# Performance work log

Measured on AMD Instinct MI355X. Metric: run time of the kernel, lower is better.

## Reference

```python
import math
import jax, jax.numpy as jnp
import numpy as np

B, C, H, W, R, P = 4, 64, 128, 128, 5, 8


def circular_sample(x, r):
    """Bilinear ring sampling, grid_sample(align_corners=True, padding_mode='zeros') equivalent.
    x: [B,C,H,W]; returns [B,H,W,C,P]."""
    Bx, Cx, Hx, Wx = x.shape
    angles = jnp.linspace(0.0, 2.0 * math.pi, P + 1)[:-1]
    di = r * jnp.sin(angles)  # row offsets [P]
    dj = r * jnp.cos(angles)  # col offsets [P]
    yy = jnp.arange(Hx, dtype=x.dtype)[:, None, None] + di[None, None, :]  # [H,1,P]
    xx = jnp.arange(Wx, dtype=x.dtype)[None, :, None] + dj[None, None, :]  # [1,W,P]
    yy = jnp.broadcast_to(yy, (Hx, Wx, P))
    xx = jnp.broadcast_to(xx, (Hx, Wx, P))
    y0 = jnp.floor(yy); x0 = jnp.floor(xx)
    wy = yy - y0; wx = xx - x0
    y0i = y0.astype(jnp.int32); x0i = x0.astype(jnp.int32)

    def gather(yi, xi):
        valid = ((yi >= 0) & (yi < Hx) & (xi >= 0) & (xi < Wx)).astype(x.dtype)
        yc = jnp.clip(yi, 0, Hx - 1)
        xc = jnp.clip(xi, 0, Wx - 1)
        return x[:, :, yc, xc] * valid  # [B,C,H,W,P], zeros padding

    v00 = gather(y0i, x0i)
    v01 = gather(y0i, x0i + 1)
    v10 = gather(y0i + 1, x0i)
    v11 = gather(y0i + 1, x0i + 1)
    out = (v00 * (1 - wy) * (1 - wx) + v01 * (1 - wy) * wx
           + v10 * wy * (1 - wx) + v11 * wy * wx)
    return jnp.transpose(out, (0, 2, 3, 1, 4))  # [B,H,W,C,P] -> channel-major, point-minor


def setup_inputs() -> dict:
    key = jax.random.key(0)
    ks = jax.random.split(key, 3)
    x = jax.random.normal(ks[0], (B, C, H, W), dtype=jnp.float32)
    CP = C * P
    W1 = jax.random.normal(ks[1], (R, CP, 64), dtype=jnp.float32) / np.sqrt(CP)
    b1 = jnp.zeros((R, 64), dtype=jnp.float32)
    g1 = jnp.ones((R, 64), dtype=jnp.float32)
    bt1 = jnp.zeros((R, 64), dtype=jnp.float32)
    W2 = jax.random.normal(ks[2], (R, 64, C), dtype=jnp.float32) / 8.0
    b2 = jnp.zeros((R, C), dtype=jnp.float32)
    return {"x": x, "W1": W1, "b1": b1, "g1": g1, "bt1": bt1, "W2": W2, "b2": b2}


def reference(x, W1, b1, g1, bt1, W2, b2):
    Bx, Cx, Hx, Wx = x.shape
    acc = jnp.zeros((Bx, Hx * Wx, Cx), dtype=x.dtype)
    for r in range(R):  # small fixed radius loop, matches module structure
        feat = circular_sample(x, float(r)).reshape(Bx, Hx * Wx, Cx * P)
        h = feat @ W1[r] + b1[r]
        mu = jnp.mean(h, axis=-1, keepdims=True)
        var = jnp.mean((h - mu) ** 2, axis=-1, keepdims=True)
        h = (h - mu) / jnp.sqrt(var + 1e-5) * g1[r] + bt1[r]
        h = jax.nn.gelu(h, approximate=False)  # torch nn.GELU default = exact erf
        acc = acc + h @ W2[r] + b2[r]
    wts = jax.nn.sigmoid(acc).reshape(Bx, Hx, Wx, Cx).transpose(0, 3, 1, 2)
    return x * wts
```

## Files before the change

### kernel.cpp

```cpp
#include <hip/hip_runtime.h>
#include <math.h>

namespace {
constexpr int Hh = 128, Ww = 128;
constexpr int NDCAP = 48;
constexpr int UROW  = 56;

using short8 = __attribute__((ext_vector_type(8))) short;
using f32x4  = __attribute__((ext_vector_type(4))) float;

__device__ __forceinline__ unsigned short f2bf(float f) {
    union { float f; unsigned int u; } v; v.f = f;
    unsigned int u = v.u;
    unsigned int r = (u + 0x7FFFu + ((u >> 16) & 1u)) >> 16;
    return (unsigned short)r;
}

union U8 { unsigned int d[4]; short8 s; };

constexpr size_t XBF_OFF  = 0;
constexpr size_t W1P_OFF  = 8388608;
constexpr size_t W2P_OFF  = W1P_OFF + (size_t)484 * 4096;
constexpr size_t META_OFF = W2P_OFF + 40960;
constexpr size_t UOFF_OFF = META_OFF + 64;
constexpr size_t WVEC_OFF = UOFF_OFF + 1152;
constexpr size_t WS_NEED  = WVEC_OFF + 7680;
}

__global__ void rrf_table(int* __restrict__ meta, int* __restrict__ uoff,
                          float* __restrict__ wvec)
{
    __shared__ float grid[5][81][8];
    __shared__ unsigned char keep[5][81];
    __shared__ short dofs[5][81];
    __shared__ int nds[5];

    const int t = threadIdx.x;
    for (int i = t; i < 5 * 81 * 8; i += 512) ((float*)grid)[i] = 0.f;
    for (int i = t; i < 5 * UROW; i += 512) uoff[i] = 0;
    __syncthreads();

    if (t < 40) {
        int r = t >> 3, p = t & 7;
        float ang = (float)p * 0.78539818525314331f;
        float si = (float)sin((double)ang);
        float co = (float)cos((double)ang);
        float di = (float)r * si;
        float dj = (float)r * co;
        float y0f = floorf(di), x0f = floorf(dj);
        float wy = di - y0f, wx = dj - x0f;
        int y0 = (int)y0f, x0 = (int)x0f;
        float tw[4] = {(1.f - wy) * (1.f - wx), (1.f - wy) * wx,
                       wy * (1.f - wx), wy * wx};
        int ty[4] = {y0, y0, y0 + 1, y0 + 1};
        int tx[4] = {x0, x0 + 1, x0, x0 + 1};
        #pragma unroll
        for (int q = 0; q < 4; ++q) {
            if (fabsf(tw[q]) < 1e-6f) continue;
            grid[r][(ty[q] + 4) * 9 + (tx[q] + 4)][p] = tw[q];
        }
    }
    __syncthreads();

    if (t < 405) {
        int r = t / 81, ci = t - r * 81;
        float mx = 0.f;
        #pragma unroll
        for (int p = 0; p < 8; ++p) mx = fmaxf(mx, fabsf(grid[r][ci][p]));
        keep[r][ci] = (mx > 1e-6f) ? 1 : 0;
    }
    __syncthreads();

    if (t < 5) {
        int nd = 0;
        for (int ci = 0; ci < 81; ++ci) {
            dofs[t][ci] = (short)nd;
            nd += keep[t][ci];
        }
        nds[t] = nd;
    }
    __syncthreads();

    if (t < 405) {
        int r = t / 81, ci = t - r * 81;
        if (keep[r][ci]) {
            int d = dofs[r][ci];
            int iy = ci / 9, ix = ci - iy * 9;
            uoff[r * UROW + d] = (iy * 24 + (ix - 4)) * 80;
            #pragma unroll
            for (int p = 0; p < 8; ++p)
                wvec[(r * NDCAP + d) * 8 + p] = grid[r][ci][p];
        }
    }
    if (t == 0) {
        int base = 0;
        for (int r = 0; r < 5; ++r) {
            int nd  = nds[r];
            int ndp = (nd + 3) & ~3;
            meta[r]      = ndp;
            meta[5 + r]  = base;
            meta[11 + r] = nd;
            base += ndp;
        }
        meta[10] = base;
    }
}

__global__ void rrf_pack(const float* __restrict__ W1, const float* __restrict__ W2,
                         const int* __restrict__ meta, const float* __restrict__ wvec,
                         unsigned short* __restrict__ w1p, unsigned short* __restrict__ w2p)
{
    int bb = blockIdx.x;
    if (bb < 480) {
        int gid  = bb * 256 + threadIdx.x;
        int lane = gid & 63;
        int t    = (gid >> 6) & 3;
        int cc   = (gid >> 8) & 1;
        int rd   = gid >> 9;
        int r = rd / NDCAP, d = rd % NDCAP;
        if (r >= 5 || d >= meta[r]) return;
        int TOTP  = meta[10];
        int chunk = cc * TOTP + meta[5 + r] + d;
        unsigned short* dst = w1p + ((size_t)(chunk * 4 + t) * 64 + lane) * 8;
        if (d >= meta[11 + r]) {
            short8 z = {0,0,0,0,0,0,0,0};
            *(short8*)dst = z;
            return;
        }
        int n = t * 16 + (lane & 15);
        int cbase = cc * 32 + ((lane >> 4) << 3);
        const float* wv  = wvec + (r * NDCAP + d) * 8;
        const float* w1r = W1 + (size_t)r * 512 * 64;
        short8 o;
        #pragma unroll
        for (int j = 0; j < 8; ++j) {
            int c = cbase + j;
            float acc = 0.f;
            #pragma unroll
            for (int p = 0; p < 8; ++p)
                acc = fmaf(wv[p], w1r[(c * 8 + p) * 64 + n], acc);
            o[j] = (short)f2bf(acc);
        }
        *(short8*)dst = o;
    } else {
        int i = (bb - 480) * 256 + threadIdx.x;
        if (i < 20480) {
            int j    = i & 7;
            int lane = (i >> 3) & 63;
            int kc2  = (i >> 9) & 1;
            int t    = (i >> 10) & 3;
            int r    = i >> 12;
            int n = kc2 * 32 + ((lane >> 4) << 3) + j;
            int m = t * 16 + (lane & 15);
            w2p[i] = f2bf(W2[(r * 64 + n) * 64 + m]);
        }
    }
}

__global__ void rrf_xpose(const float* __restrict__ x, unsigned short* __restrict__ xbf)
{
    __shared__ float tl[64][65];
    int b   = blockIdx.x >> 8;
    int px0 = (blockIdx.x & 255) * 64;
    int tx = threadIdx.x & 63, ty = threadIdx.x >> 6;
    #pragma unroll
    for (int i = 0; i < 16; ++i) {
        int c = i * 4 + ty;
        tl[c][tx] = x[(((size_t)b * 64 + c) << 14) + px0 + tx];
    }
    __syncthreads();
    #pragma unroll
    for (int i = 0; i < 16; ++i) {
        int px = i * 4 + ty;
        xbf[(((size_t)b << 14) + px0 + px) * 64 + tx] = f2bf(tl[tx][px]);
    }
}

#define LDA(K, CI) { const unsigned short* _q = ap + (size_t)(CI) * 2048 + (lane << 3);   \
    A##K[0] = *(const short8*)(_q);        A##K[1] = *(const short8*)(_q + 512);          \
    A##K[2] = *(const short8*)(_q + 1024); A##K[3] = *(const short8*)(_q + 1536); }

#define LDB(K, U) {                                                                       \
    B##K[0] = *(const short8*)(tb + ((U) + lb0));                                         \
    B##K[1] = *(const short8*)(tb + ((U) + lb1)); }

#define MF(K) {                                                                           \
    _Pragma("unroll")                                                                     \
    for (int _t = 0; _t < 4; ++_t) {                                                      \
        hv[_t][0] = __builtin_amdgcn_mfma_f32_16x16x32_bf16(A##K[_t], B##K[0], hv[_t][0], 0, 0, 0); \
        hv[_t][1] = __builtin_amdgcn_mfma_f32_16x16x32_bf16(A##K[_t], B##K[1], hv[_t][1], 0, 0, 0); \
    } }

__global__ __launch_bounds__(512, 2)
void rrf_stencil3(const float* __restrict__ x, const unsigned short* __restrict__ xbf,
                  const unsigned short* __restrict__ w1p, const unsigned short* __restrict__ w2p,
                  const int* __restrict__ meta, const int* __restrict__ uoff,
                  const float* __restrict__ b1v, const float* __restrict__ g1v,
                  const float* __restrict__ btv, const float* __restrict__ b2v,
                  float* __restrict__ out)
{
    __shared__ __align__(16) unsigned short tile[576 * 40];
    __shared__ int uo_lds[5 * UROW];
    __shared__ int meta_lds[16];

    const int tid  = threadIdx.x;
    const int w    = tid >> 6;
    const int lane = tid & 63;
    const int col  = lane & 15;
    const int g    = lane >> 4;

    const int bid = blockIdx.x;
    const int b   = bid >> 6;
    const int r0  = ((bid >> 3) & 7) * 16;
    const int c0  = (bid & 7) * 16;

    char* tb = (char*)tile;
    const int lb0 = ((2 * w + 0) * 24 + col + 4) * 80 + g * 16;
    const int lb1 = ((2 * w + 1) * 24 + col + 4) * 80 + g * 16;

    for (int s = tid; s < 5 * UROW; s += 512) uo_lds[s] = uoff[s];
    if (tid < 16) meta_lds[tid] = meta[tid];

    f32x4 acc2[4][2];
    #pragma unroll
    for (int t = 0; t < 4; ++t)
        #pragma unroll
        for (int q = 0; q < 2; ++q) acc2[t][q] = f32x4{0.f, 0.f, 0.f, 0.f};

    const int src0 = 32 * (g & 1) + col;
    const int src1 = src0 + 16;
    const bool ghi = (g >> 1) != 0;

    #pragma unroll 1
    for (int r = 0; r < 5; ++r) {
        f32x4 hv[4][2];
        #pragma unroll
        for (int t = 0; t < 4; ++t)
            #pragma unroll
            for (int q = 0; q < 2; ++q) hv[t][q] = f32x4{0.f, 0.f, 0.f, 0.f};

        #pragma unroll 1
        for (int cc = 0; cc < 2; ++cc) {
            __syncthreads();
            for (int s = tid; s < 576; s += 512) {
                int trow = s / 24, tcol = s - trow * 24;
                int row = r0 - 4 + trow, cg = c0 - 4 + tcol;
                bool valid = ((unsigned)row < 128u) && ((unsigned)cg < 128u);
                unsigned short* dst = tile + s * 40;
                if (valid) {
                    const unsigned short* src =
                        xbf + (((size_t)(b << 14)) + row * 128 + cg) * 64 + cc * 32;
                    #pragma unroll
                    for (int k = 0; k < 4; ++k)
                        *(short8*)(dst + k * 8) = *(const short8*)(src + k * 8);
                } else {
                    short8 z = {0, 0, 0, 0, 0, 0, 0, 0};
                    #pragma unroll
                    for (int k = 0; k < 4; ++k) *(short8*)(dst + k * 8) = z;
                }
            }
            __syncthreads();

            const int ndp  = __builtin_amdgcn_readfirstlane(meta_lds[r]);
            const int base = __builtin_amdgcn_readfirstlane(meta_lds[5 + r]);
            const int TOTP = __builtin_amdgcn_readfirstlane(meta_lds[10]);
            const unsigned short* ap = w1p + (size_t)(cc * TOTP + base) * 2048;
            const int* uo = uo_lds + r * UROW;

            short8 A0[4], A1[4], A2[4], A3[4];
            short8 B0[2], B1[2], B2[2], B3[2];
            LDA(0, 0) LDB(0, uo[0])
            LDA(1, 1) LDB(1, uo[1])
            LDA(2, 2) LDB(2, uo[2])
            LDA(3, 3) LDB(3, uo[3])
            int u0 = uo[4], u1 = uo[5], u2 = uo[6], u3 = uo[7];
            #pragma unroll 1
            for (int d = 0; d < ndp; d += 4) {
                MF(0) LDA(0, d + 4) LDB(0, u0)
                MF(1) LDA(1, d + 5) LDB(1, u1)
                MF(2) LDA(2, d + 6) LDB(2, u2)
                MF(3) LDA(3, d + 7) LDB(3, u3)
                u0 = uo[d + 8];  u1 = uo[d + 9];
                u2 = uo[d + 10]; u3 = uo[d + 11];
            }
        }

        float b1r[4][4], g1r[4][4], btr[4][4];
        #pragma unroll
        for (int t = 0; t < 4; ++t)
            #pragma unroll
            for (int e = 0; e < 4; ++e) {
                int n = t * 16 + g * 4 + e;
                b1r[t][e] = b1v[r * 64 + n];
                g1r[t][e] = g1v[r * 64 + n];
                btr[t][e] = btv[r * 64 + n];
            }

        #pragma unroll
        for (int q = 0; q < 2; ++q) {
            float hq[4][4];
            float s = 0.f;
            #pragma unroll
            for (int t = 0; t < 4; ++t)
                #pragma unroll
                for (int e = 0; e < 4; ++e) {
                    float v = hv[t][q][e] + b1r[t][e];
                    hq[t][e] = v;
                    s += v;
                }
            s += __shfl_xor(s, 16);
            s += __shfl_xor(s, 32);
            const float mu = s * 0.015625f;
            float s2 = 0.f;
            #pragma unroll
            for (int t = 0; t < 4; ++t)
                #pragma unroll
                for (int e = 0; e < 4; ++e) {
                    float dd = hq[t][e] - mu;
                    s2 = fmaf(dd, dd, s2);
                }
            s2 += __shfl_xor(s2, 16);
            s2 += __shfl_xor(s2, 32);
            const float rs = rsqrtf(s2 * 0.015625f + 1e-5f);

            unsigned int pk[4][2];
            #pragma unroll
            for (int t = 0; t < 4; ++t) {
                float ge[4];
                #pragma unroll
                for (int e = 0; e < 4; ++e) {
                    float v = (hq[t][e] - mu) * rs * g1r[t][e] + btr[t][e];
                    ge[e] = 0.5f * v * (1.f + erff(v * 0.70710678118654752f));
                }
                pk[t][0] = (unsigned int)f2bf(ge[0]) | ((unsigned int)f2bf(ge[1]) << 16);
                pk[t][1] = (unsigned int)f2bf(ge[2]) | ((unsigned int)f2bf(ge[3]) << 16);
            }

            #pragma unroll
            for (int kc2 = 0; kc2 < 2; ++kc2) {
                unsigned int d0a = (unsigned int)__shfl((int)pk[kc2 * 2][0],     src0);
                unsigned int d0b = (unsigned int)__shfl((int)pk[kc2 * 2 + 1][0], src0);
                unsigned int d1a = (unsigned int)__shfl((int)pk[kc2 * 2][1],     src0);
                unsigned int d1b = (unsigned int)__shfl((int)pk[kc2 * 2 + 1][1], src0);
                unsigned int d2a = (unsigned int)__shfl((int)pk[kc2 * 2][0],     src1);
                unsigned int d2b = (unsigned int)__shfl((int)pk[kc2 * 2 + 1][0], src1);
                unsigned int d3a = (unsigned int)__shfl((int)pk[kc2 * 2][1],     src1);
                unsigned int d3b = (unsigned int)__shfl((int)pk[kc2 * 2 + 1][1], src1);
                U8 u;
                u.d[0] = ghi ? d0b : d0a;
                u.d[1] = ghi ? d1b : d1a;
                u.d[2] = ghi ? d2b : d2a;
                u.d[3] = ghi ? d3b : d3a;
                const unsigned short* a2 = w2p + (size_t)r * 4096 + (size_t)lane * 8
                                         + (size_t)kc2 * 512;
                #pragma unroll
                for (int t = 0; t < 4; ++t) {
                    short8 a2f = *(const short8*)(a2 + (size_t)t * 1024);
                    acc2[t][q] = __builtin_amdgcn_mfma_f32_16x16x32_bf16(
                        a2f, u.s, acc2[t][q], 0, 0, 0);
                }
            }
        }
    }

    #pragma unroll
    for (int t = 0; t < 4; ++t) {
        #pragma unroll
        for (int e = 0; e < 4; ++e) {
            int m = t * 16 + g * 4 + e;
            float sb = b2v[m] + b2v[64 + m] + b2v[128 + m] + b2v[192 + m] + b2v[256 + m];
            #pragma unroll
            for (int q = 0; q < 2; ++q) {
                float a = acc2[t][q][e] + sb;
                float wts = 1.f / (1.f + expf(-a));
                size_t off = (((size_t)b * 64 + m) << 14)
                           + (size_t)(r0 + 2 * w + q) * 128 + (c0 + col);
                out[off] = x[off] * wts;
            }
        }
    }
}

__global__ void rrf_prepack(const float* __restrict__ W1, const float* __restrict__ W2,
                            unsigned short* __restrict__ w1p, unsigned short* __restrict__ w2p)
{
    int i = blockIdx.x * 256 + threadIdx.x;
    if (i < 163840) {
        int jq   = i & 7;
        int lane = (i >> 3) & 63;
        int kc   = (i >> 9) & 15;
        int t    = (i >> 13) & 3;
        int r    = i >> 15;
        int k = kc * 32 + ((lane >> 4) << 3) + jq;
        int n = t * 16 + (lane & 15);
        w1p[i] = f2bf(W1[(r * 512 + k) * 64 + n]);
    }
    if (i < 20480) {
        int jq   = i & 7;
        int lane = (i >> 3) & 63;
        int kc2  = (i >> 9) & 1;
        int t    = (i >> 10) & 3;
        int r    = i >> 12;
        int n = kc2 * 32 + ((lane >> 4) << 3) + jq;
        int m = t * 16 + (lane & 15);
        w2p[i] = f2bf(W2[(r * 64 + n) * 64 + m]);
    }
}

__global__ __launch_bounds__(256, 2)
void rrf_mfma(const float* __restrict__ x,
              const unsigned short* __restrict__ w1p, const unsigned short* __restrict__ w2p,
              const float* __restrict__ b1v, const float* __restrict__ g1v,
              const float* __restrict__ btv, const float* __restrict__ b2v,
              float* __restrict__ out)
{
    __shared__ unsigned short gbuf[4][16][72];

    const int tid  = threadIdx.x;
    const int w    = tid >> 6;
    const int lane = tid & 63;
    const int col  = lane & 15;
    const int g    = lane >> 4;

    const int bid  = blockIdx.x;
    const int b    = bid >> 8;
    const int rem  = bid & 255;
    const int irow = rem >> 1;
    const int j0   = (rem & 1) * 64;
    const int j    = j0 + w * 16 + col;

    const float fi = (float)irow;
    const float fj = (float)j;
    const float* xb = x + ((size_t)b << 20);

    f32x4 acc2[4] = {f32x4{0,0,0,0}, f32x4{0,0,0,0}, f32x4{0,0,0,0}, f32x4{0,0,0,0}};

    #pragma unroll 1
    for (int r = 0; r < 5; ++r) {
        int   o00[8], o01[8], o10[8], o11[8];
        float w00[8], w01[8], w10[8], w11[8];
        const float rf = (float)r;
        #pragma unroll
        for (int p = 0; p < 8; ++p) {
            float ang = (float)p * 0.78539818525314331f;
            float yy = fi + rf * sinf(ang);
            float xx = fj + rf * cosf(ang);
            float y0f = floorf(yy), x0f = floorf(xx);
            float wy = yy - y0f, wx = xx - x0f;
            int y0 = (int)y0f, x0i = (int)x0f;
            int y1 = y0 + 1,   x1  = x0i + 1;
            float m00 = (y0 >= 0 && y0 < Hh && x0i >= 0 && x0i < Ww) ? 1.f : 0.f;
            float m01 = (y0 >= 0 && y0 < Hh && x1  >= 0 && x1  < Ww) ? 1.f : 0.f;
            float m10 = (y1 >= 0 && y1 < Hh && x0i >= 0 && x0i < Ww) ? 1.f : 0.f;
            float m11 = (y1 >= 0 && y1 < Hh && x1  >= 0 && x1  < Ww) ? 1.f : 0.f;
            int y0c = y0 < 0 ? 0 : (y0 > Hh - 1 ? Hh - 1 : y0);
            int y1c = y1 < 0 ? 0 : (y1 > Hh - 1 ? Hh - 1 : y1);
            int x0c = x0i < 0 ? 0 : (x0i > Ww - 1 ? Ww - 1 : x0i);
            int x1c = x1 < 0 ? 0 : (x1 > Ww - 1 ? Ww - 1 : x1);
            w00[p] = (1.f - wy) * (1.f - wx) * m00;
            w01[p] = (1.f - wy) * wx * m01;
            w10[p] = wy * (1.f - wx) * m10;
            w11[p] = wy * wx * m11;
            o00[p] = (y0c * Ww + x0c) * 4;
            o01[p] = (y0c * Ww + x1c) * 4;
            o10[p] = (y1c * Ww + x0c) * 4;
            o11[p] = (y1c * Ww + x1c) * 4;
        }

        f32x4 hv[4] = {f32x4{0,0,0,0}, f32x4{0,0,0,0}, f32x4{0,0,0,0}, f32x4{0,0,0,0}};
        const unsigned short* abase0 = w1p + ((size_t)((r * 64) * 64 + lane)) * 8;
        #pragma unroll 2
        for (int kc = 0; kc < 16; ++kc) {
            const int c = (kc << 2) + g;
            const char* xp = (const char*)(xb + ((size_t)c << 14));
            short8 bfrag;
            #pragma unroll
            for (int p = 0; p < 8; ++p) {
                float v00 = *(const float*)(xp + o00[p]);
                float v01 = *(const float*)(xp + o01[p]);
                float v10 = *(const float*)(xp + o10[p]);
                float v11 = *(const float*)(xp + o11[p]);
                float v = w00[p] * v00;
                v = fmaf(w01[p], v01, v);
                v = fmaf(w10[p], v10, v);
                v = fmaf(w11[p], v11, v);
                bfrag[p] = (short)f2bf(v);
            }
            const unsigned short* ab = abase0 + (size_t)kc * 512;
            #pragma unroll
            for (int t = 0; t < 4; ++t) {
                short8 af = *(const short8*)(ab + (size_t)t * 8192);
                hv[t] = __builtin_amdgcn_mfma_f32_16x16x32_bf16(af, bfrag, hv[t], 0, 0, 0);
            }
        }

        const int nb = g << 2;
        float hq[4][4];
        float s = 0.f;
        #pragma unroll
        for (int t = 0; t < 4; ++t)
            #pragma unroll
            for (int q = 0; q < 4; ++q) {
                float hvq = hv[t][q] + b1v[r * 64 + t * 16 + nb + q];
                hq[t][q] = hvq;
                s += hvq;
            }
        s += __shfl_xor(s, 16);
        s += __shfl_xor(s, 32);
        const float mu = s * 0.015625f;
        float s2 = 0.f;
        #pragma unroll
        for (int t = 0; t < 4; ++t)
            #pragma unroll
            for (int q = 0; q < 4; ++q) {
                float d = hq[t][q] - mu;
                s2 = fmaf(d, d, s2);
            }
        s2 += __shfl_xor(s2, 16);
        s2 += __shfl_xor(s2, 32);
        const float rs = rsqrtf(s2 * 0.015625f + 1e-5f);

        #pragma unroll
        for (int t = 0; t < 4; ++t)
            #pragma unroll
            for (int q = 0; q < 4; ++q) {
                int n = t * 16 + nb + q;
                float v = (hq[t][q] - mu) * rs * g1v[r * 64 + n] + btv[r * 64 + n];
                hq[t][q] = 0.5f * v * (1.f + erff(v * 0.70710678118654752f));
            }
        #pragma unroll
        for (int t = 0; t < 4; ++t) {
            #pragma unroll
            for (int q2 = 0; q2 < 4; q2 += 2) {
                unsigned int u = (unsigned int)f2bf(hq[t][q2])
                               | ((unsigned int)f2bf(hq[t][q2 + 1]) << 16);
                *(unsigned int*)&gbuf[w][col][t * 16 + nb + q2] = u;
            }
        }

        const unsigned short* a2base = w2p + ((size_t)((r * 8) * 64 + lane)) * 8;
        #pragma unroll
        for (int kc2 = 0; kc2 < 2; ++kc2) {
            short8 bf2 = *(const short8*)&gbuf[w][col][kc2 * 32 + g * 8];
            const unsigned short* a2 = a2base + (size_t)kc2 * 512;
            #pragma unroll
            for (int t = 0; t < 4; ++t) {
                short8 a2f = *(const short8*)(a2 + (size_t)t * 1024);
                acc2[t] = __builtin_amdgcn_mfma_f32_16x16x32_bf16(a2f, bf2, acc2[t], 0, 0, 0);
            }
        }
    }

    #pragma unroll
    for (int t = 0; t < 4; ++t) {
        #pragma unroll
        for (int q = 0; q < 4; ++q) {
            int m = t * 16 + (g << 2) + q;
            float sb = b2v[m] + b2v[64 + m] + b2v[128 + m] + b2v[192 + m] + b2v[256 + m];
            float a = acc2[t][q] + sb;
            float wts = 1.f / (1.f + expf(-a));
            size_t off = (((size_t)b * 64 + m) << 14) + ((size_t)irow << 7) + j;
            out[off] = x[off] * wts;
        }
    }
}

extern "C" void kernel_launch(void* const* d_in, const int* in_sizes, int n_in,
                              void* d_out, int out_size, void* d_ws, size_t ws_size,
                              hipStream_t stream)
{
    const float* x  = (const float*)d_in[0];
    const float* W1 = (const float*)d_in[1];
    const float* b1 = (const float*)d_in[2];
    const float* g1 = (const float*)d_in[3];
    const float* bt = (const float*)d_in[4];
    const float* W2 = (const float*)d_in[5];
    const float* b2 = (const float*)d_in[6];
    float* outp = (float*)d_out;
    char* ws = (char*)d_ws;

    if (ws_size >= WS_NEED) {
        unsigned short* xbf = (unsigned short*)(ws + XBF_OFF);
        unsigned short* w1p = (unsigned short*)(ws + W1P_OFF);
        unsigned short* w2p = (unsigned short*)(ws + W2P_OFF);
        int*   meta  = (int*)(ws + META_OFF);
        int*   uoffp = (int*)(ws + UOFF_OFF);
        float* wvec  = (float*)(ws + WVEC_OFF);

        rrf_xpose<<<dim3(1024), dim3(256), 0, stream>>>(x, xbf);
        rrf_table<<<dim3(1), dim3(512), 0, stream>>>(meta, uoffp, wvec);
        rrf_pack<<<dim3(564), dim3(256), 0, stream>>>(W1, W2, meta, wvec, w1p, w2p);
        rrf_stencil3<<<dim3(256), dim3(512), 0, stream>>>(x, xbf, w1p, w2p, meta, uoffp,
                                                          b1, g1, bt, b2, outp);
    } else {
        unsigned short* w1p = (unsigned short*)d_ws;
        unsigned short* w2p = w1p + 163840;
        rrf_prepack<<<dim3(640), dim3(256), 0, stream>>>(W1, W2, w1p, w2p);
        rrf_mfma<<<dim3(1024), dim3(256), 0, stream>>>(x, w1p, w2p, b1, g1, bt, b2, outp);
    }
}
```

Before: 108.5 us.

## Split hidden dim across wave pairs, load both channel halves once, LDS GELU exchange

The stencil kernel now assigns each wave 4 pixel rows and half of the 64 hidden units, instead of 2 rows and all 64 units. Each W1 fragment is reused across 4 B tiles, which lowers per-wave global weight traffic. Both 32-channel halves of the input tile are loaded into LDS once up front, removing the per-radius reload and its barriers. LayerNorm statistics are combined across the wave pair through LDS using single-pass sum and sum-of-squares, and GELU outputs pass through an LDS buffer instead of lane shuffles. In exchange it uses more LDS, adds barriers per radius, and the E[x²]−mu² variance is less numerically robust.

New measurement: 98.65 us. -9.1%, faster.

```diff
diff --git a/kernel.cpp b/kernel.cpp
--- a/kernel.cpp
+++ b/kernel.cpp
@@ -15,8 +15,6 @@
     unsigned int r = (u + 0x7FFFu + ((u >> 16) & 1u)) >> 16;
     return (unsigned short)r;
 }
-
-union U8 { unsigned int d[4]; short8 s; };
 
 constexpr size_t XBF_OFF  = 0;
 constexpr size_t W1P_OFF  = 8388608;
@@ -176,30 +174,33 @@
     }
 }
 
-#define LDA(K, CI) { const unsigned short* _q = ap + (size_t)(CI) * 2048 + (lane << 3);   \
-    A##K[0] = *(const short8*)(_q);        A##K[1] = *(const short8*)(_q + 512);          \
-    A##K[2] = *(const short8*)(_q + 1024); A##K[3] = *(const short8*)(_q + 1536); }
-
-#define LDB(K, U) {                                                                       \
+#define LDA4(K, CI) { const unsigned short* _q = ap + (size_t)(CI) * 2048 + tpoff + (lane << 3); \
+    A##K[0] = *(const short8*)(_q); A##K[1] = *(const short8*)(_q + 512); }
+
+#define LDB4(K, U) {                                                                      \
     B##K[0] = *(const short8*)(tb + ((U) + lb0));                                         \
-    B##K[1] = *(const short8*)(tb + ((U) + lb1)); }
-
-#define MF(K) {                                                                           \
+    B##K[1] = *(const short8*)(tb + ((U) + lb1));                                         \
+    B##K[2] = *(const short8*)(tb + ((U) + lb2));                                         \
+    B##K[3] = *(const short8*)(tb + ((U) + lb3)); }
+
+#define MF4(K) {                                                                          \
     _Pragma("unroll")                                                                     \
-    for (int _t = 0; _t < 4; ++_t) {                                                      \
-        hv[_t][0] = __builtin_amdgcn_mfma_f32_16x16x32_bf16(A##K[_t], B##K[0], hv[_t][0], 0, 0, 0); \
-        hv[_t][1] = __builtin_amdgcn_mfma_f32_16x16x32_bf16(A##K[_t], B##K[1], hv[_t][1], 0, 0, 0); \
+    for (int _q = 0; _q < 4; ++_q) {                                                      \
+        hv[0][_q] = __builtin_amdgcn_mfma_f32_16x16x32_bf16(A##K[0], B##K[_q], hv[0][_q], 0, 0, 0); \
+        hv[1][_q] = __builtin_amdgcn_mfma_f32_16x16x32_bf16(A##K[1], B##K[_q], hv[1][_q], 0, 0, 0); \
     } }
 
 __global__ __launch_bounds__(512, 2)
-void rrf_stencil3(const float* __restrict__ x, const unsigned short* __restrict__ xbf,
+void rrf_stencil4(const float* __restrict__ x, const unsigned short* __restrict__ xbf,
                   const unsigned short* __restrict__ w1p, const unsigned short* __restrict__ w2p,
                   const int* __restrict__ meta, const int* __restrict__ uoff,
                   const float* __restrict__ b1v, const float* __restrict__ g1v,
                   const float* __restrict__ btv, const float* __restrict__ b2v,
                   float* __restrict__ out)
 {
-    __shared__ __align__(16) unsigned short tile[576 * 40];
+    __shared__ __align__(16) unsigned short tile[2][23040];
+    __shared__ __align__(16) unsigned short gbuf[16][16][72];
+    __shared__ float wsum[2][4][4][16][2];
     __shared__ int uo_lds[5 * UROW];
     __shared__ int meta_lds[16];
 
@@ -208,157 +209,171 @@
     const int lane = tid & 63;
     const int col  = lane & 15;
     const int g    = lane >> 4;
+    const int tp   = w & 1;
+    const int rq   = w >> 1;
+    const int tpoff = tp * 1024;
 
     const int bid = blockIdx.x;
     const int b   = bid >> 6;
     const int r0  = ((bid >> 3) & 7) * 16;
     const int c0  = (bid & 7) * 16;
 
-    char* tb = (char*)tile;
-    const int lb0 = ((2 * w + 0) * 24 + col + 4) * 80 + g * 16;
-    const int lb1 = ((2 * w + 1) * 24 + col + 4) * 80 + g * 16;
+    const int lb0 = ((4 * rq + 0) * 24 + col + 4) * 80 + g * 16;
+    const int lb1 = ((4 * rq + 1) * 24 + col + 4) * 80 + g * 16;
+    const int lb2 = ((4 * rq + 2) * 24 + col + 4) * 80 + g * 16;
+    const int lb3 = ((4 * rq + 3) * 24 + col + 4) * 80 + g * 16;
 
     for (int s = tid; s < 5 * UROW; s += 512) uo_lds[s] = uoff[s];
     if (tid < 16) meta_lds[tid] = meta[tid];
 
-    f32x4 acc2[4][2];
+    for (int s = tid; s < 576; s += 512) {
+        int trow = s / 24, tcol = s - trow * 24;
+        int row = r0 - 4 + trow, cg = c0 - 4 + tcol;
+        bool valid = ((unsigned)row < 128u) && ((unsigned)cg < 128u);
+        unsigned short* d0 = &tile[0][s * 40];
+        unsigned short* d1 = &tile[1][s * 40];
+        if (valid) {
+            const unsigned short* src =
+                xbf + (((size_t)(b << 14)) + row * 128 + cg) * 64;
+            #pragma unroll
+            for (int k = 0; k < 4; ++k) {
+                *(short8*)(d0 + k * 8) = *(const short8*)(src + k * 8);
+                *(short8*)(d1 + k * 8) = *(const short8*)(src + 32 + k * 8);
+            }
+        } else {
+            short8 z = {0, 0, 0, 0, 0, 0, 0, 0};
+            #pragma unroll
+            for (int k = 0; k < 4; ++k) {
+                *(short8*)(d0 + k * 8) = z;
+                *(short8*)(d1 + k * 8) = z;
+            }
+        }
+    }
+    __syncthreads();
+
+    f32x4 acc2[4][4];
     #pragma unroll
     for (int t = 0; t < 4; ++t)
         #pragma unroll
-        for (int q = 0; q < 2; ++q) acc2[t][q] = f32x4{0.f, 0.f, 0.f, 0.f};
-
-    const int src0 = 32 * (g & 1) + col;
-    const int src1 = src0 + 16;
-    const bool ghi = (g >> 1) != 0;
+        for (int q = 0; q < 4; ++q) acc2[t][q] = f32x4{0.f, 0.f, 0.f, 0.f};
 
     #pragma unroll 1
     for (int r = 0; r < 5; ++r) {
-        f32x4 hv[4][2];
-        #pragma unroll
-        for (int t = 0; t < 4; ++t)
-            #pragma unroll
-            for (int q = 0; q < 2; ++q) hv[t][q] = f32x4{0.f, 0.f, 0.f, 0.f};
+        f32x4 hv[2][4];
+        #pragma unroll
+        for (int t = 0; t < 2; ++t)
+            #pragma unroll
+            for (int q = 0; q < 4; ++q) hv[t][q] = f32x4{0.f, 0.f, 0.f, 0.f};
+
+        const int ndp  = __builtin_amdgcn_readfirstlane(meta_lds[r]);
+        const int base = __builtin_amdgcn_readfirstlane(meta_lds[5 + r]);
+        const int TOTP = __builtin_amdgcn_readfirstlane(meta_lds[10]);
+        const int* uo = uo_lds + r * UROW;
 
         #pragma unroll 1
         for (int cc = 0; cc < 2; ++cc) {
-            __syncthreads();
-            for (int s = tid; s < 576; s += 512) {
-                int trow = s / 24, tcol = s - trow * 24;
-                int row = r0 - 4 + trow, cg = c0 - 4 + tcol;
-                bool valid = ((unsigned)row < 128u) && ((unsigned)cg < 128u);
-                unsigned short* dst = tile + s * 40;
-                if (valid) {
-                    const unsigned short* src =
-                        xbf + (((size_t)(b << 14)) + row * 128 + cg) * 64 + cc * 32;
-                    #pragma unroll
-                    for (int k = 0; k < 4; ++k)
-                        *(short8*)(dst + k * 8) = *(const short8*)(src + k * 8);
-                } else {
-                    short8 z = {0, 0, 0, 0, 0, 0, 0, 0};
-                    #pragma unroll
-                    for (int k = 0; k < 4; ++k) *(short8*)(dst + k * 8) = z;
-                }
-            }
-            __syncthreads();
-
-            const int ndp  = __builtin_amdgcn_readfirstlane(meta_lds[r]);
-            const int base = __builtin_amdgcn_readfirstlane(meta_lds[5 + r]);
-            const int TOTP = __builtin_amdgcn_readfirstlane(meta_lds[10]);
             const unsigned short* ap = w1p + (size_t)(cc * TOTP + base) * 2048;
-            const int* uo = uo_lds + r * UROW;
-
-            short8 A0[4], A1[4], A2[4], A3[4];
-            short8 B0[2], B1[2], B2[2], B3[2];
-            LDA(0, 0) LDB(0, uo[0])
-            LDA(1, 1) LDB(1, uo[1])
-            LDA(2, 2) LDB(2, uo[2])
-            LDA(3, 3) LDB(3, uo[3])
+            const char* tb = (const char*)(&tile[cc][0]);
+
+            short8 A0[2], A1[2], A2[2], A3[2];
+            short8 B0[4], B1[4], B2[4], B3[4];
+            LDA4(0, 0) LDB4(0, uo[0])
+            LDA4(1, 1) LDB4(1, uo[1])
+            LDA4(2, 2) LDB4(2, uo[2])
+            LDA4(3, 3) LDB4(3, uo[3])
             int u0 = uo[4], u1 = uo[5], u2 = uo[6], u3 = uo[7];
             #pragma unroll 1
             for (int d = 0; d < ndp; d += 4) {
-                MF(0) LDA(0, d + 4) LDB(0, u0)
-                MF(1) LDA(1, d + 5) LDB(1, u1)
-                MF(2) LDA(2, d + 6) LDB(2, u2)
-                MF(3) LDA(3, d + 7) LDB(3, u3)
+                MF4(0) LDA4(0, d + 4) LDB4(0, u0)
+                MF4(1) LDA4(1, d + 5) LDB4(1, u1)
+                MF4(2) LDA4(2, d + 6) LDB4(2, u2)
+                MF4(3) LDA4(3, d + 7) LDB4(3, u3)
                 u0 = uo[d + 8];  u1 = uo[d + 9];
                 u2 = uo[d + 10]; u3 = uo[d + 11];
             }
         }
 
-        float b1r[4][4], g1r[4][4], btr[4][4];
-        #pragma unroll
-        for (int t = 0; t < 4; ++t)
+        float b1r[2][4], g1r[2][4], btr[2][4];
+        #pragma unroll
+        for (int t = 0; t < 2; ++t)
             #pragma unroll
             for (int e = 0; e < 4; ++e) {
-                int n = t * 16 + g * 4 + e;
+                int n = (2 * tp + t) * 16 + g * 4 + e;
                 b1r[t][e] = b1v[r * 64 + n];
                 g1r[t][e] = g1v[r * 64 + n];
                 btr[t][e] = btv[r * 64 + n];
             }
 
-        #pragma unroll
-        for (int q = 0; q < 2; ++q) {
-            float hq[4][4];
-            float s = 0.f;
-            #pragma unroll
-            for (int t = 0; t < 4; ++t)
+        float hq[2][4][4];
+        float sA[4], sB[4];
+        #pragma unroll
+        for (int q = 0; q < 4; ++q) {
+            float s = 0.f, s2 = 0.f;
+            #pragma unroll
+            for (int t = 0; t < 2; ++t)
                 #pragma unroll
                 for (int e = 0; e < 4; ++e) {
                     float v = hv[t][q][e] + b1r[t][e];
-                    hq[t][e] = v;
+                    hq[t][q][e] = v;
                     s += v;
+                    s2 = fmaf(v, v, s2);
                 }
-            s += __shfl_xor(s, 16);
-            s += __shfl_xor(s, 32);
-            const float mu = s * 0.015625f;
-            float s2 = 0.f;
-            #pragma unroll
-            for (int t = 0; t < 4; ++t)
-                #pragma unroll
-                for (int e = 0; e < 4; ++e) {
-                    float dd = hq[t][e] - mu;
-                    s2 = fmaf(dd, dd, s2);
-                }
-            s2 += __shfl_xor(s2, 16);
-            s2 += __shfl_xor(s2, 32);
-            const float rs = rsqrtf(s2 * 0.015625f + 1e-5f);
-
-            unsigned int pk[4][2];
-            #pragma unroll
-            for (int t = 0; t < 4; ++t) {
+            s  += __shfl_xor(s, 16);  s  += __shfl_xor(s, 32);
+            s2 += __shfl_xor(s2, 16); s2 += __shfl_xor(s2, 32);
+            sA[q] = s; sB[q] = s2;
+        }
+        if (g == 0) {
+            #pragma unroll
+            for (int q = 0; q < 4; ++q) {
+                wsum[tp][rq][q][col][0] = sA[q];
+                wsum[tp][rq][q][col][1] = sB[q];
+            }
+        }
+        __syncthreads();
+
+        #pragma unroll
+        for (int q = 0; q < 4; ++q) {
+            float so  = wsum[tp ^ 1][rq][q][col][0];
+            float s2o = wsum[tp ^ 1][rq][q][col][1];
+            const float mu = (sA[q] + so) * 0.015625f;
+            const float ms = (sB[q] + s2o) * 0.015625f;
+            const float rs = rsqrtf(ms - mu * mu + 1e-5f);
+            const int row = 4 * rq + q;
+            #pragma unroll
+            for (int t = 0; t < 2; ++t) {
                 float ge[4];
                 #pragma unroll
                 for (int e = 0; e < 4; ++e) {
-                    float v = (hq[t][e] - mu) * rs * g1r[t][e] + btr[t][e];
+                    float v = (hq[t][q][e] - mu) * rs * g1r[t][e] + btr[t][e];
                     ge[e] = 0.5f * v * (1.f + erff(v * 0.70710678118654752f));
                 }
-                pk[t][0] = (unsigned int)f2bf(ge[0]) | ((unsigned int)f2bf(ge[1]) << 16);
-                pk[t][1] = (unsigned int)f2bf(ge[2]) | ((unsigned int)f2bf(ge[3]) << 16);
-            }
-
+                int n0 = (2 * tp + t) * 16 + g * 4;
+                *(unsigned int*)&gbuf[row][col][n0] =
+                    (unsigned int)f2bf(ge[0]) | ((unsigned int)f2bf(ge[1]) << 16);
+                *(unsigned int*)&gbuf[row][col][n0 + 2] =
+                    (unsigned int)f2bf(ge[2]) | ((unsigned int)f2bf(ge[3]) << 16);
+            }
+        }
+        __syncthreads();
+
+        const unsigned short* a2base = w2p + (size_t)r * 4096 + (size_t)lane * 8;
+        short8 a2f[2][4];
+        #pragma unroll
+        for (int kc2 = 0; kc2 < 2; ++kc2)
+            #pragma unroll
+            for (int t = 0; t < 4; ++t)
+                a2f[kc2][t] = *(const short8*)(a2base + kc2 * 512 + t * 1024);
+
+        #pragma unroll
+        for (int q = 0; q < 4; ++q) {
+            const int row = 4 * rq + q;
             #pragma unroll
             for (int kc2 = 0; kc2 < 2; ++kc2) {
-                unsigned int d0a = (unsigned int)__shfl((int)pk[kc2 * 2][0],     src0);
-                unsigned int d0b = (unsigned int)__shfl((int)pk[kc2 * 2 + 1][0], src0);
-                unsigned int d1a = (unsigned int)__shfl((int)pk[kc2 * 2][1],     src0);
-                unsigned int d1b = (unsigned int)__shfl((int)pk[kc2 * 2 + 1][1], src0);
-                unsigned int d2a = (unsigned int)__shfl((int)pk[kc2 * 2][0],     src1);
-                unsigned int d2b = (unsigned int)__shfl((int)pk[kc2 * 2 + 1][0], src1);
-                unsigned int d3a = (unsigned int)__shfl((int)pk[kc2 * 2][1],     src1);
-                unsigned int d3b = (unsigned int)__shfl((int)pk[kc2 * 2 + 1][1], src1);
-                U8 u;
-                u.d[0] = ghi ? d0b : d0a;
-                u.d[1] = ghi ? d1b : d1a;
-                u.d[2] = ghi ? d2b : d2a;
-                u.d[3] = ghi ? d3b : d3a;
-                const unsigned short* a2 = w2p + (size_t)r * 4096 + (size_t)lane * 8
-                                         + (size_t)kc2 * 512;
+                short8 bf2 = *(const short8*)&gbuf[row][col][kc2 * 32 + g * 8];
                 #pragma unroll
-                for (int t = 0; t < 4; ++t) {
-                    short8 a2f = *(const short8*)(a2 + (size_t)t * 1024);
+                for (int t = 0; t < 4; ++t)
                     acc2[t][q] = __builtin_amdgcn_mfma_f32_16x16x32_bf16(
-                        a2f, u.s, acc2[t][q], 0, 0, 0);
-                }
+                        a2f[kc2][t], bf2, acc2[t][q], 0, 0, 0);
             }
         }
     }
@@ -370,11 +385,11 @@
             int m = t * 16 + g * 4 + e;
             float sb = b2v[m] + b2v[64 + m] + b2v[128 + m] + b2v[192 + m] + b2v[256 + m];
             #pragma unroll
-            for (int q = 0; q < 2; ++q) {
+            for (int q = 0; q < 4; ++q) {
                 float a = acc2[t][q][e] + sb;
                 float wts = 1.f / (1.f + expf(-a));
                 size_t off = (((size_t)b * 64 + m) << 14)
-                           + (size_t)(r0 + 2 * w + q) * 128 + (c0 + col);
+                           + (size_t)(r0 + 4 * rq + q) * 128 + (c0 + col);
                 out[off] = x[off] * wts;
             }
         }
@@ -590,7 +605,7 @@
         rrf_xpose<<<dim3(1024), dim3(256), 0, stream>>>(x, xbf);
         rrf_table<<<dim3(1), dim3(512), 0, stream>>>(meta, uoffp, wvec);
         rrf_pack<<<dim3(564), dim3(256), 0, stream>>>(W1, W2, meta, wvec, w1p, w2p);
-        rrf_stencil3<<<dim3(256), dim3(512), 0, stream>>>(x, xbf, w1p, w2p, meta, uoffp,
+        rrf_stencil4<<<dim3(256), dim3(512), 0, stream>>>(x, xbf, w1p, w2p, meta, uoffp,
                                                           b1, g1, bt, b2, outp);
     } else {
         unsigned short* w1p = (unsigned short*)d_ws;
```
